# Performance work log

Measured on AMD Instinct MI355X. Metric: run time of the kernel, lower is better.

Reference implementation:

```python
import jax, jax.numpy as jnp
import numpy as np

N = 2_000_000
C0 = 0.28209479177387814
C1 = 0.4886025119029199


def setup_inputs() -> dict:
    key = jax.random.key(0)
    ks = jax.random.split(key, 6)
    return {
        "view_dirs": jax.random.normal(ks[0], (N, 3), dtype=jnp.float32),
        "xyz": jax.random.uniform(ks[1], (N, 3), dtype=jnp.float32) * 2.0 - 1.0,
        "scale_log": jax.random.uniform(ks[2], (N, 3), dtype=jnp.float32) - 3.0,
        "rot_quat": jax.random.uniform(ks[3], (N, 4), dtype=jnp.float32),
        "opacity_logit": jax.random.uniform(ks[4], (N, 1), dtype=jnp.float32),
        "sh_coeffs": jax.random.uniform(ks[5], (N, 3, 4), dtype=jnp.float32),
    }


def _build_rotation(q):
    # F.normalize along dim=1 with eps=1e-12
    q = q / jnp.maximum(jnp.linalg.norm(q, axis=1, keepdims=True), 1e-12)
    r, x, y, z = q[:, 0], q[:, 1], q[:, 2], q[:, 3]
    R = jnp.stack([
        1 - 2 * (y * y + z * z), 2 * (x * y - r * z), 2 * (x * z + r * y),
        2 * (x * y + r * z), 1 - 2 * (x * x + z * z), 2 * (y * z - r * x),
        2 * (x * z - r * y), 2 * (y * z + r * x), 1 - 2 * (x * x + y * y),
    ], axis=-1).reshape(-1, 3, 3)
    return R


def _eval_sh(sh_coeffs, dirs):
    # degree = 1 -> 4 coeffs
    x, y, z = dirs[:, 0:1], dirs[:, 1:2], dirs[:, 2:3]  # [N,1] broadcast over color
    return (C0 * sh_coeffs[:, :, 0]
            - C1 * y * sh_coeffs[:, :, 1]
            + C1 * z * sh_coeffs[:, :, 2]
            - C1 * x * sh_coeffs[:, :, 3])


def reference(view_dirs, xyz, scale_log, rot_quat, opacity_logit, sh_coeffs):
    opacity = jax.nn.sigmoid(opacity_logit)                  # [N,1]
    scale = jnp.exp(scale_log)                               # [N,3]
    rgb = jax.nn.sigmoid(_eval_sh(sh_coeffs, view_dirs))     # [N,3]
    R = _build_rotation(rot_quat)                            # [N,3,3]
    M = R * scale[:, None, :]                                # R @ diag(scale), columns scaled
    cov3d = jnp.einsum('nij,nkj->nik', M, M)                 # M @ M^T
    return xyz, cov3d, rgb, opacity
```

## Files before the change

### kernel.cpp

```cpp
#include <hip/hip_runtime.h>

#define C0 0.28209479177387814f
#define C1 0.4886025119029199f

__device__ __forceinline__ float sigmoidf(float x) {
    return 1.0f / (1.0f + expf(-x));
}

__global__ __launch_bounds__(256) void gauss_kernel(
    const float* __restrict__ view_dirs,
    const float* __restrict__ xyz,
    const float* __restrict__ scale_log,
    const float4* __restrict__ rot_quat,
    const float* __restrict__ opacity_logit,
    const float4* __restrict__ sh,
    float* __restrict__ out_xyz,
    float* __restrict__ out_cov,
    float* __restrict__ out_rgb,
    float* __restrict__ out_op,
    int N)
{
    int i = blockIdx.x * blockDim.x + threadIdx.x;
    if (i >= N) return;

    float vx = view_dirs[3*i+0], vy = view_dirs[3*i+1], vz = view_dirs[3*i+2];
    float px = xyz[3*i+0],       py = xyz[3*i+1],       pz = xyz[3*i+2];
    float sl0 = scale_log[3*i+0], sl1 = scale_log[3*i+1], sl2 = scale_log[3*i+2];
    float4 q  = rot_quat[i];
    float  ol = opacity_logit[i];
    float4 c0 = sh[3*i+0];
    float4 c1 = sh[3*i+1];
    float4 c2 = sh[3*i+2];

    float opacity = sigmoidf(ol);

    float r0 = C0*c0.x - C1*vy*c0.y + C1*vz*c0.z - C1*vx*c0.w;
    float r1 = C0*c1.x - C1*vy*c1.y + C1*vz*c1.z - C1*vx*c1.w;
    float r2 = C0*c2.x - C1*vy*c2.y + C1*vz*c2.z - C1*vx*c2.w;
    r0 = sigmoidf(r0); r1 = sigmoidf(r1); r2 = sigmoidf(r2);

    float nrm = sqrtf(q.x*q.x + q.y*q.y + q.z*q.z + q.w*q.w);
    float inv = 1.0f / fmaxf(nrm, 1e-12f);
    float r = q.x*inv, x = q.y*inv, y = q.z*inv, z = q.w*inv;

    float R00 = 1.0f - 2.0f*(y*y + z*z);
    float R01 = 2.0f*(x*y - r*z);
    float R02 = 2.0f*(x*z + r*y);
    float R10 = 2.0f*(x*y + r*z);
    float R11 = 1.0f - 2.0f*(x*x + z*z);
    float R12 = 2.0f*(y*z - r*x);
    float R20 = 2.0f*(x*z - r*y);
    float R21 = 2.0f*(y*z + r*x);
    float R22 = 1.0f - 2.0f*(x*x + y*y);

    float s0 = expf(sl0), s1 = expf(sl1), s2 = expf(sl2);

    float M00 = R00*s0, M01 = R01*s1, M02 = R02*s2;
    float M10 = R10*s0, M11 = R11*s1, M12 = R12*s2;
    float M20 = R20*s0, M21 = R21*s1, M22 = R22*s2;

    float cv00 = M00*M00 + M01*M01 + M02*M02;
    float cv01 = M00*M10 + M01*M11 + M02*M12;
    float cv02 = M00*M20 + M01*M21 + M02*M22;
    float cv11 = M10*M10 + M11*M11 + M12*M12;
    float cv12 = M10*M20 + M11*M21 + M12*M22;
    float cv22 = M20*M20 + M21*M21 + M22*M22;

    out_xyz[3*i+0] = px; out_xyz[3*i+1] = py; out_xyz[3*i+2] = pz;

    float* cp = out_cov + 9*i;
    cp[0] = cv00; cp[1] = cv01; cp[2] = cv02;
    cp[3] = cv01; cp[4] = cv11; cp[5] = cv12;
    cp[6] = cv02; cp[7] = cv12; cp[8] = cv22;

    out_rgb[3*i+0] = r0; out_rgb[3*i+1] = r1; out_rgb[3*i+2] = r2;
    out_op[i] = opacity;
}

extern "C" void kernel_launch(void* const* d_in, const int* in_sizes, int n_in,
                              void* d_out, int out_size, void* d_ws, size_t ws_size,
                              hipStream_t stream) {
    const float*  view_dirs     = (const float*)d_in[0];
    const float*  xyz           = (const float*)d_in[1];
    const float*  scale_log     = (const float*)d_in[2];
    const float4* rot_quat      = (const float4*)d_in[3];
    const float*  opacity_logit = (const float*)d_in[4];
    const float4* sh            = (const float4*)d_in[5];

    int N = in_sizes[4];

    float* out = (float*)d_out;
    float* out_xyz = out;
    float* out_cov = out + (size_t)3*N;
    float* out_rgb = out + (size_t)12*N;
    float* out_op  = out + (size_t)15*N;

    int block = 256;
    int grid = (N + block - 1) / block;
    gauss_kernel<<<grid, block, 0, stream>>>(view_dirs, xyz, scale_log, rot_quat,
                                             opacity_logit, sh,
                                             out_xyz, out_cov, out_rgb, out_op, N);
}
```

Baseline: 278.5 us.

## Stage strided per-element loads and stores through shared memory for coalesced float4 access

Each block cooperatively loads its slice of view_dirs, scale_log and SH coefficients into LDS with contiguous float4 reads, and copies xyz straight to the output with float4 copies. Per-thread covariance and RGB results are then staged in LDS and written back as contiguous float4 stores. This replaces stride-3 and stride-9 per-thread global accesses with fully coalesced vector transactions, at the cost of 18 KB of LDS per block, extra barriers and possible LDS bank conflicts.

```diff
diff --git a/kernel.cpp b/kernel.cpp
--- a/kernel.cpp
+++ b/kernel.cpp
@@ -2,79 +2,151 @@
 
 #define C0 0.28209479177387814f
 #define C1 0.4886025119029199f
+#define BLK 256
 
 __device__ __forceinline__ float sigmoidf(float x) {
     return 1.0f / (1.0f + expf(-x));
 }
 
-__global__ __launch_bounds__(256) void gauss_kernel(
+__global__ __launch_bounds__(BLK) void gauss_kernel(
     const float* __restrict__ view_dirs,
     const float* __restrict__ xyz,
     const float* __restrict__ scale_log,
     const float4* __restrict__ rot_quat,
     const float* __restrict__ opacity_logit,
-    const float4* __restrict__ sh,
+    const float* __restrict__ sh,
     float* __restrict__ out_xyz,
     float* __restrict__ out_cov,
     float* __restrict__ out_rgb,
     float* __restrict__ out_op,
     int N)
 {
-    int i = blockIdx.x * blockDim.x + threadIdx.x;
-    if (i >= N) return;
+    __shared__ float smem[4608];
+    float* s_vd  = smem;
+    float* s_sl  = smem + 768;
+    float* s_sh  = smem + 1536;
+    float* s_cov = smem;
+    float* s_rgb = smem + 2304;
 
-    float vx = view_dirs[3*i+0], vy = view_dirs[3*i+1], vz = view_dirs[3*i+2];
-    float px = xyz[3*i+0],       py = xyz[3*i+1],       pz = xyz[3*i+2];
-    float sl0 = scale_log[3*i+0], sl1 = scale_log[3*i+1], sl2 = scale_log[3*i+2];
-    float4 q  = rot_quat[i];
-    float  ol = opacity_logit[i];
-    float4 c0 = sh[3*i+0];
-    float4 c1 = sh[3*i+1];
-    float4 c2 = sh[3*i+2];
+    const int t  = threadIdx.x;
+    const int e0 = blockIdx.x * BLK;
+    const int nelem = min(BLK, N - e0);
+    const int n3 = 3 * nelem;
 
-    float opacity = sigmoidf(ol);
+    {
+        const float* g = xyz + (size_t)3 * e0;
+        float*       o = out_xyz + (size_t)3 * e0;
+        int nf4 = n3 >> 2;
+        for (int k = t; k < nf4; k += BLK)
+            ((float4*)o)[k] = ((const float4*)g)[k];
+        int rem = n3 & 3;
+        if (t < rem) o[nf4 * 4 + t] = g[nf4 * 4 + t];
+    }
 
-    float r0 = C0*c0.x - C1*vy*c0.y + C1*vz*c0.z - C1*vx*c0.w;
-    float r1 = C0*c1.x - C1*vy*c1.y + C1*vz*c1.z - C1*vx*c1.w;
-    float r2 = C0*c2.x - C1*vy*c2.y + C1*vz*c2.z - C1*vx*c2.w;
-    r0 = sigmoidf(r0); r1 = sigmoidf(r1); r2 = sigmoidf(r2);
+    {
+        const float* g = view_dirs + (size_t)3 * e0;
+        int nf4 = n3 >> 2;
+        for (int k = t; k < nf4; k += BLK)
+            ((float4*)s_vd)[k] = ((const float4*)g)[k];
+        int rem = n3 & 3;
+        if (t < rem) s_vd[nf4 * 4 + t] = g[nf4 * 4 + t];
+    }
+    {
+        const float* g = scale_log + (size_t)3 * e0;
+        int nf4 = n3 >> 2;
+        for (int k = t; k < nf4; k += BLK)
+            ((float4*)s_sl)[k] = ((const float4*)g)[k];
+        int rem = n3 & 3;
+        if (t < rem) s_sl[nf4 * 4 + t] = g[nf4 * 4 + t];
+    }
+    {
+        const float* g = sh + (size_t)12 * e0;
+        int nf4 = (12 * nelem) >> 2;
+        for (int k = t; k < nf4; k += BLK)
+            ((float4*)s_sh)[k] = ((const float4*)g)[k];
+    }
+    __syncthreads();
 
-    float nrm = sqrtf(q.x*q.x + q.y*q.y + q.z*q.z + q.w*q.w);
-    float inv = 1.0f / fmaxf(nrm, 1e-12f);
-    float r = q.x*inv, x = q.y*inv, y = q.z*inv, z = q.w*inv;
+    const int i = e0 + t;
+    const bool active = (t < nelem);
+    float cv[9], rgb[3], opac;
 
-    float R00 = 1.0f - 2.0f*(y*y + z*z);
-    float R01 = 2.0f*(x*y - r*z);
-    float R02 = 2.0f*(x*z + r*y);
-    float R10 = 2.0f*(x*y + r*z);
-    float R11 = 1.0f - 2.0f*(x*x + z*z);
-    float R12 = 2.0f*(y*z - r*x);
-    float R20 = 2.0f*(x*z - r*y);
-    float R21 = 2.0f*(y*z + r*x);
-    float R22 = 1.0f - 2.0f*(x*x + y*y);
+    if (active) {
+        float4 q  = rot_quat[i];
+        float  ol = opacity_logit[i];
 
-    float s0 = expf(sl0), s1 = expf(sl1), s2 = expf(sl2);
+        float vx = s_vd[3 * t + 0], vy = s_vd[3 * t + 1], vz = s_vd[3 * t + 2];
+        float sl0 = s_sl[3 * t + 0], sl1 = s_sl[3 * t + 1], sl2 = s_sl[3 * t + 2];
+        float4 c0 = ((float4*)s_sh)[3 * t + 0];
+        float4 c1 = ((float4*)s_sh)[3 * t + 1];
+        float4 c2 = ((float4*)s_sh)[3 * t + 2];
 
-    float M00 = R00*s0, M01 = R01*s1, M02 = R02*s2;
-    float M10 = R10*s0, M11 = R11*s1, M12 = R12*s2;
-    float M20 = R20*s0, M21 = R21*s1, M22 = R22*s2;
+        opac = sigmoidf(ol);
 
-    float cv00 = M00*M00 + M01*M01 + M02*M02;
-    float cv01 = M00*M10 + M01*M11 + M02*M12;
-    float cv02 = M00*M20 + M01*M21 + M02*M22;
-    float cv11 = M10*M10 + M11*M11 + M12*M12;
-    float cv12 = M10*M20 + M11*M21 + M12*M22;
-    float cv22 = M20*M20 + M21*M21 + M22*M22;
+        rgb[0] = sigmoidf(C0 * c0.x - C1 * vy * c0.y + C1 * vz * c0.z - C1 * vx * c0.w);
+        rgb[1] = sigmoidf(C0 * c1.x - C1 * vy * c1.y + C1 * vz * c1.z - C1 * vx * c1.w);
+        rgb[2] = sigmoidf(C0 * c2.x - C1 * vy * c2.y + C1 * vz * c2.z - C1 * vx * c2.w);
 
-    out_xyz[3*i+0] = px; out_xyz[3*i+1] = py; out_xyz[3*i+2] = pz;
+        float nrm = sqrtf(q.x * q.x + q.y * q.y + q.z * q.z + q.w * q.w);
+        float inv = 1.0f / fmaxf(nrm, 1e-12f);
+        float r = q.x * inv, x = q.y * inv, y = q.z * inv, z = q.w * inv;
 
-    float* cp = out_cov + 9*i;
-    cp[0] = cv00; cp[1] = cv01; cp[2] = cv02;
-    cp[3] = cv01; cp[4] = cv11; cp[5] = cv12;
-    cp[6] = cv02; cp[7] = cv12; cp[8] = cv22;
+        float R00 = 1.0f - 2.0f * (y * y + z * z);
+        float R01 = 2.0f * (x * y - r * z);
+        float R02 = 2.0f * (x * z + r * y);
+        float R10 = 2.0f * (x * y + r * z);
+        float R11 = 1.0f - 2.0f * (x * x + z * z);
+        float R12 = 2.0f * (y * z - r * x);
+        float R20 = 2.0f * (x * z - r * y);
+        float R21 = 2.0f * (y * z + r * x);
+        float R22 = 1.0f - 2.0f * (x * x + y * y);
 
-    out_rgb[3*i+0] = r0; out_rgb[3*i+1] = r1; out_rgb[3*i+2] = r2;
-    out_op[i] = opacity;
+        float s0 = expf(sl0), s1 = expf(sl1), s2 = expf(sl2);
+
+        float M00 = R00 * s0, M01 = R01 * s1, M02 = R02 * s2;
+        float M10 = R10 * s0, M11 = R11 * s1, M12 = R12 * s2;
+        float M20 = R20 * s0, M21 = R21 * s1, M22 = R22 * s2;
+
+        cv[0] = M00 * M00 + M01 * M01 + M02 * M02;
+        cv[1] = M00 * M10 + M01 * M11 + M02 * M12;
+        cv[2] = M00 * M20 + M01 * M21 + M02 * M22;
+        cv[4] = M10 * M10 + M11 * M11 + M12 * M12;
+        cv[5] = M10 * M20 + M11 * M21 + M12 * M22;
+        cv[8] = M20 * M20 + M21 * M21 + M22 * M22;
+        cv[3] = cv[1]; cv[6] = cv[2]; cv[7] = cv[5];
+
+        out_op[i] = opac;
+    }
+
+    __syncthreads();
+
+    if (active) {
+        #pragma unroll
+        for (int k = 0; k < 9; k++) s_cov[9 * t + k] = cv[k];
+        s_rgb[3 * t + 0] = rgb[0];
+        s_rgb[3 * t + 1] = rgb[1];
+        s_rgb[3 * t + 2] = rgb[2];
+    }
+
+    __syncthreads();
+
+    {
+        float* g = out_cov + (size_t)9 * e0;
+        int nfl = 9 * nelem;
+        int nf4 = nfl >> 2;
+        for (int k = t; k < nf4; k += BLK)
+            ((float4*)g)[k] = ((float4*)s_cov)[k];
+        int rem = nfl & 3;
+        if (t < rem) g[nf4 * 4 + t] = s_cov[nf4 * 4 + t];
+    }
+    {
+        float* g = out_rgb + (size_t)3 * e0;
+        int nf4 = n3 >> 2;
+        for (int k = t; k < nf4; k += BLK)
+            ((float4*)g)[k] = ((float4*)s_rgb)[k];
+        int rem = n3 & 3;
+        if (t < rem) g[nf4 * 4 + t] = s_rgb[nf4 * 4 + t];
+    }
 }
 
 extern "C" void kernel_launch(void* const* d_in, const int* in_sizes, int n_in,
@@ -85,19 +157,18 @@
     const float*  scale_log     = (const float*)d_in[2];
     const float4* rot_quat      = (const float4*)d_in[3];
     const float*  opacity_logit = (const float*)d_in[4];
-    const float4* sh            = (const float4*)d_in[5];
+    const float*  sh            = (const float*)d_in[5];
 
     int N = in_sizes[4];
 
     float* out = (float*)d_out;
     float* out_xyz = out;
-    float* out_cov = out + (size_t)3*N;
-    float* out_rgb = out + (size_t)12*N;
-    float* out_op  = out + (size_t)15*N;
+    float* out_cov = out + (size_t)3 * N;
+    float* out_rgb = out + (size_t)12 * N;
+    float* out_op  = out + (size_t)15 * N;
 
-    int block = 256;
-    int grid = (N + block - 1) / block;
-    gauss_kernel<<<grid, block, 0, stream>>>(view_dirs, xyz, scale_log, rot_quat,
-                                             opacity_logit, sh,
-                                             out_xyz, out_cov, out_rgb, out_op, N);
+    int grid = (N + BLK - 1) / BLK;
+    gauss_kernel<<<grid, BLK, 0, stream>>>(view_dirs, xyz, scale_log, rot_quat,
+                                           opacity_logit, sh,
+                                           out_xyz, out_cov, out_rgb, out_op, N);
 }
```

New measurement: 282.3 us. No clear change (+1.4%).
